# Kernel tuning notes

Measured on AMD Instinct MI355X. Metric: run time of the kernel, lower is better.

Reference implementation:

```python
import jax, jax.numpy as jnp
import numpy as np

NEG = -1e10  # matches the -10000000000.0 boundary padding in the torch code


def nw_forward(theta, A):
    """Needleman-Wunsch forward DP with softmax (logsumexp) operator.

    theta: (B, N, M) match potentials; A: (B,) gap penalty.
    Returns Vt: (B,) terminal alignment scores.
    Recursion: V[i,j] = theta[i-1,j-1] + logsumexp(A+V[i-1,j], V[i-1,j-1], A+V[i,j-1]).
    Implemented as scan over rows (i) with an inner scan over columns (j),
    which honors the sequential DP dependencies without Python loops.
    """
    B, N, M = theta.shape
    dtype = theta.dtype
    # V[0, :] row: V[0,0]=0, V[0,j]=NEG for j>=1
    row0 = jnp.full((B, M + 1), NEG, dtype).at[:, 0].set(0.0)

    def row_step(prev_row, th_row):
        # prev_row: (B, M+1) = V[i-1, 0..M]; th_row: (B, M) = theta[:, i-1, :]
        v_up = prev_row[:, 1:]     # V[i-1, j],   j = 1..M
        v_diag = prev_row[:, :-1]  # V[i-1, j-1], j = 1..M

        def col_step(v_left, inp):
            th_j, vu, vd = inp  # each (B,)
            # order (x, m, y) = (A+up, diag, A+left), matching torch stack(v1,v2,v3)
            v = jnp.stack([A + vu, vd, A + v_left], axis=-1)  # (B, 3)
            v_new = th_j + jax.nn.logsumexp(v, axis=-1)
            return v_new, v_new

        xs = (th_row.T, v_up.T, v_diag.T)  # leading axis M
        v_init = jnp.full((B,), NEG, dtype)  # V[i, 0]
        _, row_vals = jax.lax.scan(col_step, v_init, xs)  # (M, B)
        new_row = jnp.concatenate(
            [jnp.full((B, 1), NEG, dtype), row_vals.T], axis=1)  # (B, M+1)
        return new_row, None

    last_row, _ = jax.lax.scan(row_step, row0, jnp.moveaxis(theta, 1, 0))
    return last_row[:, M]  # Vt = V[:, N, M]


def setup_inputs() -> dict:
    key = jax.random.key(0)
    k1, k2 = jax.random.split(key)
    B, N, M = 32, 512, 512
    theta = jax.random.normal(k1, (B, N, M), dtype=jnp.float32)
    A = jax.random.normal(k2, (B,), dtype=jnp.float32)
    return {"theta": theta, "A": A}


def reference(theta, A):
    return nw_forward(theta, A)
```

## Files before the change

### kernel.cpp

```cpp
#include <hip/hip_runtime.h>
#include <math.h>

#define NEGV  -10000000000.0f
#define LOG2E 1.44269504088896340736f
#define LN2F  0.69314718055994530942f

typedef float f4 __attribute__((ext_vector_type(4)));

constexpr int CS    = 32;
constexpr int ROWS  = 96;
constexpr int WL    = 33;
constexpr int CHW   = ROWS * WL;
constexpr int KCMAX = 32;
constexpr int SIT   = 48;

__global__ __launch_bounds__(512, 2) void nw_kernel(
    const float* __restrict__ theta, const float* __restrict__ A,
    float* __restrict__ out, int N, int M)
{
    __shared__ float thS[8 * CHW];
    __shared__ float bndD[9 * KCMAX * CS];
    __shared__ int   flg[9 * KCMAX];

    const int tid = threadIdx.x;
    const int w   = tid >> 6;
    const int l   = tid & 63;
    const int j   = tid;
    const int b   = blockIdx.x;
    const int NW  = blockDim.x >> 6;

    for (int i = tid; i < 9 * KCMAX; i += blockDim.x) flg[i] = 0;
    __syncthreads();

    const float a2 = A[b] * LOG2E;
    const float* __restrict__ thb = theta + (size_t)b * N * M;
    const int NM = N * M;

    const int T  = N + M - 1;
    const int KC = (T + CS - 1) / CS;
    const int wstart = 64 * w;
    const int wend   = 64 * w + 63 + N - 1;
    const int ca = wstart / CS;
    const int cb = min(KC - 1, wend / CS);

    const int srow = l >> 5;
    const int sq   = l & 31;
    const int lanebase = srow * (M - 1) + 64 * w + 63 + sq;
    const int wrbase   = w * CHW + srow * WL + sq;
    const int rdbase   = w * CHW + (63 - l) * WL;

    auto stage_load = [&](int cn, float* stg) {
        const int rb = CS * cn - 64 * w - 63;
        if (rb >= 0 && rb + (ROWS - 1) <= N - 1) {
            const float* p = thb + (size_t)rb * M;
            #pragma unroll
            for (int it = 0; it < SIT; ++it) { stg[it] = p[lanebase]; p += 2 * (M - 1); }
        } else {
            const int rbM = rb * M;
            #pragma unroll
            for (int it = 0; it < SIT; ++it) {
                int off = rbM + lanebase + it * 2 * (M - 1);
                off = min(max(off, 0), NM - 1);
                stg[it] = thb[off];
            }
        }
    };
    auto stage_write = [&](const float* stg) {
        #pragma unroll
        for (int it = 0; it < SIT; ++it) thS[wrbase + it * 2 * WL] = stg[it] * LOG2E;
    };
    auto wait_flag = [&](int idx) {
        if (__atomic_load_n(&flg[idx], __ATOMIC_ACQUIRE) == 0) {
            do { __builtin_amdgcn_s_sleep(1); }
            while (__atomic_load_n(&flg[idx], __ATOMIC_ACQUIRE) == 0);
        }
    };

    float v_prev = NEGV;
    float v_diag = (j == 0) ? 0.0f : NEGV;
    float bcarry = NEGV;

    {
        float s0[SIT];
        stage_load(ca, s0);
        stage_write(s0);
        __asm__ volatile("s_waitcnt lgkmcnt(0)" ::: "memory");
    }
    if (w > 0) {
        wait_flag(w * KCMAX + (ca - 1));
        bcarry = bndD[(w * KCMAX + ca - 1) * CS + (CS - 1)];
    }

    float stg[SIT];
    bool have = (ca + 1 <= cb);
    if (have) stage_load(ca + 1, stg);

    for (int c = ca; c <= cb; ++c) {
        float th[CS];
        #pragma unroll
        for (int k = 0; k < 8; ++k) th[k] = thS[rdbase + k * (WL + 1)];

        const bool need_bv = (w > 0) && (CS * c <= 64 * w + N - 1);
        float bv[CS];
        if (need_bv) {
            wait_flag(w * KCMAX + c);
            const f4* src = (const f4*)&bndD[(w * KCMAX + c) * CS];
            #pragma unroll
            for (int q = 0; q < CS / 4; ++q) {
                f4 t = src[q];
                bv[4*q+0] = t.x; bv[4*q+1] = t.y; bv[4*q+2] = t.z; bv[4*q+3] = t.w;
            }
        } else {
            #pragma unroll
            for (int k = 0; k < CS; ++k) bv[k] = NEGV;
        }

        #pragma unroll
        for (int k = 8; k < CS; ++k) th[k] = thS[rdbase + k * (WL + 1)];

        float res[CS];
        const bool full = (CS * c >= 64 * w + 63) &&
                          (CS * c + CS - 1 <= 64 * w + N - 1);
        if (full) {
            #pragma unroll
            for (int k = 0; k < CS; ++k) {
                float bk = (k == 0) ? bcarry : bv[k - 1];
                float vl = __int_as_float(__builtin_amdgcn_update_dpp(
                    __float_as_int(bk), __float_as_int(v_prev),
                    0x138 , 0xF, 0xF, false));
                float x = a2 + v_prev;
                float z = a2 + vl;
                float m = fmaxf(fmaxf(x, v_diag), z);
                float s = __builtin_amdgcn_exp2f(x - m)
                        + __builtin_amdgcn_exp2f(v_diag - m)
                        + __builtin_amdgcn_exp2f(z - m);
                float v = th[k] + m + __builtin_amdgcn_logf(s);
                res[k] = v;
                v_diag = vl;
                v_prev = v;
            }
        } else {
            const int tmj = CS * c - j;
            #pragma unroll
            for (int k = 0; k < CS; ++k) {
                float bk = (k == 0) ? bcarry : bv[k - 1];
                float vl = __int_as_float(__builtin_amdgcn_update_dpp(
                    __float_as_int(bk), __float_as_int(v_prev),
                    0x138, 0xF, 0xF, false));
                float x = a2 + v_prev;
                float z = a2 + vl;
                float m = fmaxf(fmaxf(x, v_diag), z);
                float s = __builtin_amdgcn_exp2f(x - m)
                        + __builtin_amdgcn_exp2f(v_diag - m)
                        + __builtin_amdgcn_exp2f(z - m);
                float v = th[k] + m + __builtin_amdgcn_logf(s);
                int dt = tmj + k;
                float vn = ((unsigned)dt < (unsigned)N) ? v
                                                        : (dt < 0 ? NEGV : v_prev);
                res[k] = vn;
                v_diag = vl;
                v_prev = vn;
            }
        }

        if (w < NW - 1 && l == 63) {
            f4* dst = (f4*)&bndD[((w + 1) * KCMAX + c) * CS];
            #pragma unroll
            for (int q = 0; q < CS / 4; ++q)
                dst[q] = (f4){res[4*q+0], res[4*q+1], res[4*q+2], res[4*q+3]};
            __atomic_store_n(&flg[(w + 1) * KCMAX + c], 1, __ATOMIC_RELEASE);
        }
        bcarry = bv[CS - 1];

        if (have) stage_write(stg);
        have = (c + 2 <= cb);
        if (have) stage_load(c + 2, stg);
        __asm__ volatile("s_waitcnt lgkmcnt(0)" ::: "memory");
    }

    if (j == M - 1) out[b] = v_prev * LN2F;
}

extern "C" void kernel_launch(void* const* d_in, const int* in_sizes, int n_in,
                              void* d_out, int out_size, void* d_ws, size_t ws_size,
                              hipStream_t stream) {
    const float* theta = (const float*)d_in[0];
    const float* A     = (const float*)d_in[1];
    float* out = (float*)d_out;

    const int B  = in_sizes[1];
    const int NM = in_sizes[0] / B;
    int N = 1;
    while (N * N < NM) N <<= 1;
    const int M = NM / N;

    hipLaunchKernelGGL(nw_kernel, dim3(B), dim3(M), 0, stream,
                       theta, A, out, N, M);
}
```

Before: 179.1 us.

## Carry DP values as (max, scale) pairs to take log off the critical path

Each cell value is now represented as a log-domain offset plus a linear scale factor (mx, s), so the recurrence propagates mn and sn = fma combinations of neighbor scales instead of computing log at every step before the next cell can start. The log is still computed per cell but only feeds the boundary output, not the serial dependency chain. A second DPP shuffle moves the scale across lanes, and once per chunk the scales are renormalised by folding their exponent into the offset to avoid overflow or underflow. This adds extra VALU work (another DPP, more FMAs, selects) and relies on the scales staying in float range within a 32-step chunk.

```diff
diff --git a/kernel.cpp b/kernel.cpp
--- a/kernel.cpp
+++ b/kernel.cpp
@@ -76,8 +76,8 @@
         }
     };
 
-    float v_prev = NEGV;
-    float v_diag = (j == 0) ? 0.0f : NEGV;
+    float mp = NEGV, sp = 1.0f;
+    float md = (j == 0) ? 0.0f : NEGV, sd = 1.0f;
     float bcarry = NEGV;
 
     {
@@ -124,42 +124,51 @@
         if (full) {
             #pragma unroll
             for (int k = 0; k < CS; ++k) {
-                float bk = (k == 0) ? bcarry : bv[k - 1];
-                float vl = __int_as_float(__builtin_amdgcn_update_dpp(
-                    __float_as_int(bk), __float_as_int(v_prev),
+                float bm = (k == 0) ? bcarry : bv[k - 1];
+                float ml = __int_as_float(__builtin_amdgcn_update_dpp(
+                    __float_as_int(bm), __float_as_int(mp),
                     0x138 , 0xF, 0xF, false));
-                float x = a2 + v_prev;
-                float z = a2 + vl;
-                float m = fmaxf(fmaxf(x, v_diag), z);
-                float s = __builtin_amdgcn_exp2f(x - m)
-                        + __builtin_amdgcn_exp2f(v_diag - m)
-                        + __builtin_amdgcn_exp2f(z - m);
-                float v = th[k] + m + __builtin_amdgcn_logf(s);
-                res[k] = v;
-                v_diag = vl;
-                v_prev = v;
+                float sl = __int_as_float(__builtin_amdgcn_update_dpp(
+                    0x3f800000 , __float_as_int(sp),
+                    0x138, 0xF, 0xF, false));
+                float u  = a2 + mp;
+                float ul = a2 + ml;
+                float mx = fmaxf(fmaxf(u, md), ul);
+                float e1 = __builtin_amdgcn_exp2f(u  - mx);
+                float e2 = __builtin_amdgcn_exp2f(md - mx);
+                float e3 = __builtin_amdgcn_exp2f(ul - mx);
+                float sn = fmaf(sl, e3, fmaf(sd, e2, sp * e1));
+                float mn = th[k] + mx;
+                res[k] = mn + __builtin_amdgcn_logf(sn);
+                md = ml; sd = sl;
+                mp = mn; sp = sn;
             }
         } else {
             const int tmj = CS * c - j;
             #pragma unroll
             for (int k = 0; k < CS; ++k) {
-                float bk = (k == 0) ? bcarry : bv[k - 1];
-                float vl = __int_as_float(__builtin_amdgcn_update_dpp(
-                    __float_as_int(bk), __float_as_int(v_prev),
+                float bm = (k == 0) ? bcarry : bv[k - 1];
+                float ml = __int_as_float(__builtin_amdgcn_update_dpp(
+                    __float_as_int(bm), __float_as_int(mp),
                     0x138, 0xF, 0xF, false));
-                float x = a2 + v_prev;
-                float z = a2 + vl;
-                float m = fmaxf(fmaxf(x, v_diag), z);
-                float s = __builtin_amdgcn_exp2f(x - m)
-                        + __builtin_amdgcn_exp2f(v_diag - m)
-                        + __builtin_amdgcn_exp2f(z - m);
-                float v = th[k] + m + __builtin_amdgcn_logf(s);
+                float sl = __int_as_float(__builtin_amdgcn_update_dpp(
+                    0x3f800000, __float_as_int(sp),
+                    0x138, 0xF, 0xF, false));
+                float u  = a2 + mp;
+                float ul = a2 + ml;
+                float mx = fmaxf(fmaxf(u, md), ul);
+                float e1 = __builtin_amdgcn_exp2f(u  - mx);
+                float e2 = __builtin_amdgcn_exp2f(md - mx);
+                float e3 = __builtin_amdgcn_exp2f(ul - mx);
+                float sn = fmaf(sl, e3, fmaf(sd, e2, sp * e1));
+                float mn = th[k] + mx;
                 int dt = tmj + k;
-                float vn = ((unsigned)dt < (unsigned)N) ? v
-                                                        : (dt < 0 ? NEGV : v_prev);
-                res[k] = vn;
-                v_diag = vl;
-                v_prev = vn;
+                bool act = (unsigned)dt < (unsigned)N;
+                float mq = act ? mn : (dt < 0 ? NEGV : mp);
+                float sq2 = act ? sn : (dt < 0 ? 1.0f : sp);
+                res[k] = mq + __builtin_amdgcn_logf(sq2);
+                md = ml; sd = sl;
+                mp = mq; sp = sq2;
             }
         }
 
@@ -171,6 +180,17 @@
             __atomic_store_n(&flg[(w + 1) * KCMAX + c], 1, __ATOMIC_RELEASE);
         }
         bcarry = bv[CS - 1];
+
+        {
+            int bs = __float_as_int(sp);
+            int ex = ((bs >> 23) & 0xff) - 127;
+            sp = __int_as_float(bs - (ex << 23));
+            mp += (float)ex;
+            int bd = __float_as_int(sd);
+            int ed = ((bd >> 23) & 0xff) - 127;
+            sd = __int_as_float(bd - (ed << 23));
+            md += (float)ed;
+        }
 
         if (have) stage_write(stg);
         have = (c + 2 <= cb);
@@ -178,7 +198,8 @@
         __asm__ volatile("s_waitcnt lgkmcnt(0)" ::: "memory");
     }
 
-    if (j == M - 1) out[b] = v_prev * LN2F;
+    if (j == M - 1)
+        out[b] = (mp + __builtin_amdgcn_logf(sp)) * LN2F;
 }
 
 extern "C" void kernel_launch(void* const* d_in, const int* in_sizes, int n_in,
```

New measurement: 178.7 us. Within noise of the previous version (-0.2%).

## Split each batch element across two workgroups with global-memory boundary handoff

Applied to the files above, without the earlier changes.

Each batch element's wavefront pipeline now spans two 256-thread workgroups instead of one 512-thread block, giving 64 blocks in place of 32. The halves exchange the column-256 boundary through agent-scope atomics and flags in a workspace buffer, which is zeroed with a memset before launch. The aim is to spread the work over more compute units and to cut per-block LDS so it can run at lower occupancy. The cost is higher latency on the cross-block handoff through L2. There is also a risk of deadlock if the second-half block is scheduled but the first half never gets to run, and the extra memset adds launch overhead.

```diff
diff --git a/kernel.cpp b/kernel.cpp
--- a/kernel.cpp
+++ b/kernel.cpp
@@ -14,43 +14,45 @@
 constexpr int KCMAX = 32;
 constexpr int SIT   = 48;
 
-__global__ __launch_bounds__(512, 2) void nw_kernel(
+__global__ __launch_bounds__(256, 1) void nw_kernel(
     const float* __restrict__ theta, const float* __restrict__ A,
-    float* __restrict__ out, int N, int M)
+    float* __restrict__ out, int* __restrict__ flagsG,
+    float* __restrict__ dataG, int N, int M)
 {
-    __shared__ float thS[8 * CHW];
-    __shared__ float bndD[9 * KCMAX * CS];
-    __shared__ int   flg[9 * KCMAX];
+    __shared__ float thS[4 * CHW];
+    __shared__ float bndL[4 * KCMAX * CS];
+    __shared__ int   flgL[4 * KCMAX];
 
     const int tid = threadIdx.x;
-    const int w   = tid >> 6;
+    const int wl  = tid >> 6;
     const int l   = tid & 63;
-    const int j   = tid;
-    const int b   = blockIdx.x;
-    const int NW  = blockDim.x >> 6;
-
-    for (int i = tid; i < 9 * KCMAX; i += blockDim.x) flg[i] = 0;
+    const int h   = blockIdx.x & 1;
+    const int b   = blockIdx.x >> 1;
+    const int W   = 4 * h + wl;
+    const int j   = 256 * h + tid;
+
+    for (int i = tid; i < 4 * KCMAX; i += blockDim.x) flgL[i] = 0;
     __syncthreads();
 
     const float a2 = A[b] * LOG2E;
     const float* __restrict__ thb = theta + (size_t)b * N * M;
     const int NM = N * M;
+    int* __restrict__ gflag   = flagsG + b * KCMAX;
+    float* __restrict__ gdata = dataG + (size_t)b * KCMAX * CS;
 
     const int T  = N + M - 1;
     const int KC = (T + CS - 1) / CS;
-    const int wstart = 64 * w;
-    const int wend   = 64 * w + 63 + N - 1;
-    const int ca = wstart / CS;
-    const int cb = min(KC - 1, wend / CS);
+    const int ca = 2 * W;
+    const int cb = min(KC - 1, (64 * W + 63 + N - 1) / CS);
 
     const int srow = l >> 5;
     const int sq   = l & 31;
-    const int lanebase = srow * (M - 1) + 64 * w + 63 + sq;
-    const int wrbase   = w * CHW + srow * WL + sq;
-    const int rdbase   = w * CHW + (63 - l) * WL;
+    const int lanebase = srow * (M - 1) + 64 * W + 63 + sq;
+    const int wrbase   = wl * CHW + srow * WL + sq;
+    const int rdbase   = wl * CHW + (63 - l) * WL;
 
     auto stage_load = [&](int cn, float* stg) {
-        const int rb = CS * cn - 64 * w - 63;
+        const int rb = CS * cn - 64 * W - 63;
         if (rb >= 0 && rb + (ROWS - 1) <= N - 1) {
             const float* p = thb + (size_t)rb * M;
             #pragma unroll
@@ -69,10 +71,18 @@
         #pragma unroll
         for (int it = 0; it < SIT; ++it) thS[wrbase + it * 2 * WL] = stg[it] * LOG2E;
     };
-    auto wait_flag = [&](int idx) {
-        if (__atomic_load_n(&flg[idx], __ATOMIC_ACQUIRE) == 0) {
+    auto wait_flag_lds = [&](int idx) {
+        if (__atomic_load_n(&flgL[idx], __ATOMIC_ACQUIRE) == 0) {
             do { __builtin_amdgcn_s_sleep(1); }
-            while (__atomic_load_n(&flg[idx], __ATOMIC_ACQUIRE) == 0);
+            while (__atomic_load_n(&flgL[idx], __ATOMIC_ACQUIRE) == 0);
+        }
+    };
+    auto wait_flag_glb = [&](int c) {
+        if (__hip_atomic_load(&gflag[c], __ATOMIC_ACQUIRE,
+                              __HIP_MEMORY_SCOPE_AGENT) == 0) {
+            do { __builtin_amdgcn_s_sleep(2); }
+            while (__hip_atomic_load(&gflag[c], __ATOMIC_ACQUIRE,
+                                     __HIP_MEMORY_SCOPE_AGENT) == 0);
         }
     };
 
@@ -86,29 +96,48 @@
         stage_write(s0);
         __asm__ volatile("s_waitcnt lgkmcnt(0)" ::: "memory");
     }
-    if (w > 0) {
-        wait_flag(w * KCMAX + (ca - 1));
-        bcarry = bndD[(w * KCMAX + ca - 1) * CS + (CS - 1)];
+    if (W > 0) {
+        const int cp = ca - 1;
+        if (wl > 0) {
+            wait_flag_lds(wl * KCMAX + cp);
+            bcarry = bndL[(wl * KCMAX + cp) * CS + (CS - 1)];
+        } else {
+            wait_flag_glb(cp);
+            bcarry = __hip_atomic_load(&gdata[cp * CS + (CS - 1)],
+                                       __ATOMIC_RELAXED, __HIP_MEMORY_SCOPE_AGENT);
+        }
     }
 
     float stg[SIT];
     bool have = (ca + 1 <= cb);
     if (have) stage_load(ca + 1, stg);
+
+    const bool pub = (W < 7);
 
     for (int c = ca; c <= cb; ++c) {
         float th[CS];
         #pragma unroll
         for (int k = 0; k < 8; ++k) th[k] = thS[rdbase + k * (WL + 1)];
 
-        const bool need_bv = (w > 0) && (CS * c <= 64 * w + N - 1);
+        const bool need_bv = (W > 0) && (CS * c <= 64 * W + N - 1);
         float bv[CS];
         if (need_bv) {
-            wait_flag(w * KCMAX + c);
-            const f4* src = (const f4*)&bndD[(w * KCMAX + c) * CS];
-            #pragma unroll
-            for (int q = 0; q < CS / 4; ++q) {
-                f4 t = src[q];
-                bv[4*q+0] = t.x; bv[4*q+1] = t.y; bv[4*q+2] = t.z; bv[4*q+3] = t.w;
+            if (wl > 0) {
+                wait_flag_lds(wl * KCMAX + c);
+                const f4* src = (const f4*)&bndL[(wl * KCMAX + c) * CS];
+                #pragma unroll
+                for (int q = 0; q < CS / 4; ++q) {
+                    f4 t = src[q];
+                    bv[4*q+0] = t.x; bv[4*q+1] = t.y;
+                    bv[4*q+2] = t.z; bv[4*q+3] = t.w;
+                }
+            } else {
+                wait_flag_glb(c);
+                #pragma unroll
+                for (int k = 0; k < CS; ++k)
+                    bv[k] = __hip_atomic_load(&gdata[c * CS + k],
+                                              __ATOMIC_RELAXED,
+                                              __HIP_MEMORY_SCOPE_AGENT);
             }
         } else {
             #pragma unroll
@@ -119,8 +148,8 @@
         for (int k = 8; k < CS; ++k) th[k] = thS[rdbase + k * (WL + 1)];
 
         float res[CS];
-        const bool full = (CS * c >= 64 * w + 63) &&
-                          (CS * c + CS - 1 <= 64 * w + N - 1);
+        const bool full = (CS * c >= 64 * W + 63) &&
+                          (CS * c + CS - 1 <= 64 * W + N - 1);
         if (full) {
             #pragma unroll
             for (int k = 0; k < CS; ++k) {
@@ -163,12 +192,21 @@
             }
         }
 
-        if (w < NW - 1 && l == 63) {
-            f4* dst = (f4*)&bndD[((w + 1) * KCMAX + c) * CS];
-            #pragma unroll
-            for (int q = 0; q < CS / 4; ++q)
-                dst[q] = (f4){res[4*q+0], res[4*q+1], res[4*q+2], res[4*q+3]};
-            __atomic_store_n(&flg[(w + 1) * KCMAX + c], 1, __ATOMIC_RELEASE);
+        if (pub && l == 63) {
+            if (wl < 3) {
+                f4* dst = (f4*)&bndL[((wl + 1) * KCMAX + c) * CS];
+                #pragma unroll
+                for (int q = 0; q < CS / 4; ++q)
+                    dst[q] = (f4){res[4*q+0], res[4*q+1], res[4*q+2], res[4*q+3]};
+                __atomic_store_n(&flgL[(wl + 1) * KCMAX + c], 1, __ATOMIC_RELEASE);
+            } else {
+                #pragma unroll
+                for (int k = 0; k < CS; ++k)
+                    __hip_atomic_store(&gdata[c * CS + k], res[k],
+                                       __ATOMIC_RELAXED, __HIP_MEMORY_SCOPE_AGENT);
+                __hip_atomic_store(&gflag[c], 1,
+                                   __ATOMIC_RELEASE, __HIP_MEMORY_SCOPE_AGENT);
+            }
         }
         bcarry = bv[CS - 1];
 
@@ -194,6 +232,10 @@
     while (N * N < NM) N <<= 1;
     const int M = NM / N;
 
-    hipLaunchKernelGGL(nw_kernel, dim3(B), dim3(M), 0, stream,
-                       theta, A, out, N, M);
+    int*   flagsG = (int*)d_ws;
+    float* dataG  = (float*)((char*)d_ws + (size_t)B * KCMAX * sizeof(int));
+    hipMemsetAsync(d_ws, 0, (size_t)B * KCMAX * sizeof(int), stream);
+
+    hipLaunchKernelGGL(nw_kernel, dim3(2 * B), dim3(256), 0, stream,
+                       theta, A, out, flagsG, dataG, N, M);
 }
```

Measured after the change: 203.2 us. 1.13x slower.
